# Optimization experiments

Hardware: AMD Instinct MI355X
Metric: run time of the kernel (lower is better)

The kernel has to match this reference:

```python
import jax, jax.numpy as jnp
import numpy as np

GROUPS = 8
EPS = 1e-5


def group_norm_dim1(x, gamma, beta):
    # Faithful to torch: GroupNorm treats dim 1 (height) as the channel axis.
    B, H, W, C = x.shape
    xg = x.reshape(B, GROUPS, H // GROUPS, W, C)
    mean = xg.mean(axis=(2, 3, 4), keepdims=True)
    var = xg.var(axis=(2, 3, 4), keepdims=True)
    xn = ((xg - mean) * jax.lax.rsqrt(var + EPS)).reshape(B, H, W, C)
    return xn * gamma[None, :, None, None] + beta[None, :, None, None]


def setup_inputs() -> dict:
    key = jax.random.key(0)
    ks = jax.random.split(key, 8)
    B, H, W, C = 4, 64, 64, 64  # height must equal units for GroupNorm to apply
    s = 1.0 / np.sqrt(C)
    return {
        "x": jax.random.normal(ks[0], (B, H, W, C), dtype=jnp.float32),
        "gamma": jnp.ones((C,), jnp.float32),
        "beta": jnp.zeros((C,), jnp.float32),
        "Wq": jax.random.normal(ks[1], (C, C), jnp.float32) * s,
        "bq": jnp.zeros((C,), jnp.float32),
        "Wk": jax.random.normal(ks[2], (C, C), jnp.float32) * s,
        "bk": jnp.zeros((C,), jnp.float32),
        "Wv": jax.random.normal(ks[3], (C, C), jnp.float32) * s,
        "bv": jnp.zeros((C,), jnp.float32),
        "Wo": jax.random.normal(ks[4], (C, C), jnp.float32) * s,
        "bo": jnp.zeros((C,), jnp.float32),
    }


def reference(x, gamma, beta, Wq, bq, Wk, bk, Wv, bv, Wo, bo):
    B, H, W, C = x.shape
    scale = C ** (-0.5)
    xn = group_norm_dim1(x, gamma, beta)
    q = xn @ Wq + bq
    k = xn @ Wk + bk
    v = xn @ Wv + bv
    # full spatial self-attention: scores [B, H, W, H*W]
    scores = jnp.einsum('bhwc,bijc->bhwij', q, k) * scale
    attn = jax.nn.softmax(scores.reshape(B, H, W, H * W), axis=-1)
    attn = attn.reshape(B, H, W, H, W)
    proj = jnp.einsum('bhwij,bijc->bhwc', attn, v)
    proj = proj @ Wo + bo
    return xn + proj
```

## Files before the change

### kernel.cpp

```cpp
#include <hip/hip_runtime.h>

typedef __bf16 bf16_t;
typedef bf16_t bf16x8 __attribute__((ext_vector_type(8)));
typedef bf16_t bf16x4 __attribute__((ext_vector_type(4)));
typedef short  short4v __attribute__((ext_vector_type(4)));
typedef float  f32x4  __attribute__((ext_vector_type(4)));

#define MFMA32(a, b, c) __builtin_amdgcn_mfma_f32_16x16x32_bf16(a, b, c, 0, 0, 0)
#define MFMA16(a, b, c) __builtin_amdgcn_mfma_f32_16x16x16bf16_1k(a, b, c, 0, 0, 0)

__global__ __launch_bounds__(256) void gn1w_kernel(const float* __restrict__ x,
    float2* __restrict__ partials,
    const float* __restrict__ Wq, const float* __restrict__ Wk,
    const float* __restrict__ Wv, const float* __restrict__ Wo,
    bf16_t* __restrict__ Wt) {
  int blk = blockIdx.x, t = threadIdx.x;
  if (blk >= 256) {
    int idx = (blk - 256) * 256 + t;
    int wsel = idx >> 12, rem = idx & 4095;
    int c = rem >> 6, kk = rem & 63;
    const float* src = (wsel == 0) ? Wq : ((wsel == 1) ? Wk : ((wsel == 2) ? Wv : Wo));
    Wt[idx] = (bf16_t)src[kk * 64 + c];
    return;
  }
  const float4* x4 = (const float4*)x + (size_t)blk * 1024;
  float s = 0.f, sq = 0.f;
  #pragma unroll
  for (int u = 0; u < 4; ++u) {
    float4 v = x4[u * 256 + t];
    s  += v.x + v.y + v.z + v.w;
    sq += v.x * v.x + v.y * v.y + v.z * v.z + v.w * v.w;
  }
  for (int off = 32; off; off >>= 1) {
    s  += __shfl_down(s, off, 64);
    sq += __shfl_down(sq, off, 64);
  }
  __shared__ float2 ps[4];
  if ((t & 63) == 0) ps[t >> 6] = make_float2(s, sq);
  __syncthreads();
  if (t == 0) {
    float S = 0.f, Q = 0.f;
    #pragma unroll
    for (int i = 0; i < 4; ++i) { S += ps[i].x; Q += ps[i].y; }
    partials[blk] = make_float2(S, Q);
  }
}

__global__ __launch_bounds__(256) void gnqkv_kernel(
    const float* __restrict__ x, const float* __restrict__ gamma,
    const float* __restrict__ beta, const float2* __restrict__ parts,
    const bf16_t* __restrict__ Wt,
    const float* __restrict__ bq, const float* __restrict__ bk, const float* __restrict__ bv,
    bf16_t* __restrict__ xnb, bf16_t* __restrict__ qo, bf16_t* __restrict__ ko,
    bf16_t* __restrict__ vo) {
  __shared__ __align__(16) bf16_t xl[4096];
  int blk = blockIdx.x, t = threadIdx.x;
  int grp = blk >> 3;
  float S = 0.f, Q = 0.f;
  #pragma unroll
  for (int i = 0; i < 8; ++i) { float2 p = parts[grp * 8 + i]; S += p.x; Q += p.y; }
  float mean = S * (1.f / 32768.f);
  float rstd = rsqrtf(Q * (1.f / 32768.f) - mean * mean + 1e-5f);
  int h = blk & 63;
  float ga = gamma[h] * rstd;
  float be = beta[h] - mean * ga;
  {
    int r = t >> 2, col0 = (t & 3) * 16;
    const float4* x4 = (const float4*)(x + (size_t)blk * 4096 + r * 64 + col0);
    bf16x8 pk0, pk1;
    float4 v0 = x4[0], v1 = x4[1], v2 = x4[2], v3 = x4[3];
    pk0[0] = (bf16_t)(v0.x * ga + be); pk0[1] = (bf16_t)(v0.y * ga + be);
    pk0[2] = (bf16_t)(v0.z * ga + be); pk0[3] = (bf16_t)(v0.w * ga + be);
    pk0[4] = (bf16_t)(v1.x * ga + be); pk0[5] = (bf16_t)(v1.y * ga + be);
    pk0[6] = (bf16_t)(v1.z * ga + be); pk0[7] = (bf16_t)(v1.w * ga + be);
    pk1[0] = (bf16_t)(v2.x * ga + be); pk1[1] = (bf16_t)(v2.y * ga + be);
    pk1[2] = (bf16_t)(v2.z * ga + be); pk1[3] = (bf16_t)(v2.w * ga + be);
    pk1[4] = (bf16_t)(v3.x * ga + be); pk1[5] = (bf16_t)(v3.y * ga + be);
    pk1[6] = (bf16_t)(v3.z * ga + be); pk1[7] = (bf16_t)(v3.w * ga + be);
    *(bf16x8*)&xnb[(size_t)blk * 4096 + r * 64 + col0]     = pk0;
    *(bf16x8*)&xnb[(size_t)blk * 4096 + r * 64 + col0 + 8] = pk1;
    int sw = r & 7, j0 = (t & 3) * 2;
    *(bf16x8*)&xl[r * 64 + ((j0 ^ sw) << 3)]       = pk0;
    *(bf16x8*)&xl[r * 64 + (((j0 + 1) ^ sw) << 3)] = pk1;
  }
  __syncthreads();
  int w = t >> 6, lane = t & 63, quad = lane >> 4, l16 = lane & 15;
  int rl = w * 16 + l16, sw2 = rl & 7;
  bf16x8 a0 = *(const bf16x8*)&xl[rl * 64 + ((quad ^ sw2) << 3)];
  bf16x8 a1 = *(const bf16x8*)&xl[rl * 64 + (((quad + 4) ^ sw2) << 3)];
  int m0 = blk * 64 + w * 16;
  int bi = m0 >> 12, kk0 = (m0 & 4095) + quad * 4;
  f32x4 zero = {0.f, 0.f, 0.f, 0.f};
  const float QSCALE = 0.125f * 1.44269504088896340736f;
  #pragma unroll
  for (int outk = 0; outk < 3; ++outk) {
    const bf16_t* wt = Wt + outk * 4096;
    const float* bias = (outk == 0) ? bq : ((outk == 1) ? bk : bv);
    #pragma unroll
    for (int nt = 0; nt < 4; ++nt) {
      int col = nt * 16 + l16;
      bf16x8 b0 = *(const bf16x8*)&wt[col * 64 + quad * 8];
      bf16x8 b1 = *(const bf16x8*)&wt[col * 64 + 32 + quad * 8];
      f32x4 acc = MFMA32(a0, b0, zero);
      acc = MFMA32(a1, b1, acc);
      float bb = bias[col];
      if (outk == 2) {
        bf16x4 pk;
        #pragma unroll
        for (int r = 0; r < 4; ++r) pk[r] = (bf16_t)(acc[r] + bb);
        *(bf16x4*)&vo[(size_t)bi * 262144 + (size_t)(kk0 >> 2) * 256 + col * 4] = pk;
      } else {
        #pragma unroll
        for (int r = 0; r < 4; ++r) {
          int m = m0 + quad * 4 + r;
          float v = acc[r] + bb;
          if (outk == 0) qo[(size_t)m * 64 + col] = (bf16_t)(v * QSCALE);
          else           ko[(size_t)m * 64 + col] = (bf16_t)v;
        }
      }
    }
  }
}

__global__ __launch_bounds__(256, 4) void flash_kernel(
    const bf16_t* __restrict__ q, const bf16_t* __restrict__ k,
    const bf16_t* __restrict__ vp, bf16_t* __restrict__ Opb, float* __restrict__ ml) {
  __shared__ float redO[2][2048];
  __shared__ float redL[2][128];
  int t = threadIdx.x;
  int w = t >> 6, lane = t & 63, quad = lane >> 4, l16 = lane & 15;
  int b = blockIdx.y, sp = blockIdx.z;
  int q0 = blockIdx.x * 32;

  bf16x8 qf[2][2];
  {
    const bf16_t* qp = q + ((size_t)b * 4096 + q0 + l16) * 64;
    #pragma unroll
    for (int qt = 0; qt < 2; ++qt)
      #pragma unroll
      for (int hh = 0; hh < 2; ++hh)
        qf[qt][hh] = *(const bf16x8*)&qp[qt * 1024 + hh * 32 + quad * 8];
  }
  f32x4 o[2][4];
  f32x4 zero = {0.f, 0.f, 0.f, 0.f};
  #pragma unroll
  for (int qt = 0; qt < 2; ++qt)
    #pragma unroll
    for (int ct = 0; ct < 4; ++ct) o[qt][ct] = zero;
  float rs[2] = {0.f, 0.f};

  const bf16_t* kbase = k  + (size_t)b * 262144;
  const bf16_t* vbase = vp + (size_t)b * 262144;
  int key00 = sp * 1024 + w * 256;

  bf16x8 kfA[2][2], kfB[2][2];
  #pragma unroll
  for (int kt = 0; kt < 2; ++kt)
    #pragma unroll
    for (int hh = 0; hh < 2; ++hh)
      kfA[kt][hh] = *(const bf16x8*)&kbase[(size_t)(key00 + kt * 16 + l16) * 64 + hh * 32 + quad * 8];

#define FLASH_STEP(KF, KEY0, PRE, KFN, PKEY)                                          \
  {                                                                                   \
    short4v va[4][2];                                 \
    _Pragma("unroll")                                                                 \
    for (int kt = 0; kt < 2; ++kt) {                                                  \
      int cb = (((KEY0) + kt * 16) >> 2) + quad;                                      \
      _Pragma("unroll")                                                               \
      for (int ct = 0; ct < 4; ++ct)                                                  \
        va[ct][kt] = *(const short4v*)&vbase[(size_t)cb * 256 + (ct * 16 + l16) * 4]; \
    }                                                                                 \
    if (PRE) {                                            \
      _Pragma("unroll")                                                               \
      for (int kt = 0; kt < 2; ++kt)                                                  \
        _Pragma("unroll")                                                             \
        for (int hh = 0; hh < 2; ++hh)                                                \
          KFN[kt][hh] = *(const bf16x8*)&kbase[(size_t)((PKEY) + kt * 16 + l16) * 64 + hh * 32 + quad * 8]; \
    }                                                                                 \
    _Pragma("unroll")                                                                 \
    for (int kt = 0; kt < 2; ++kt) {                                                  \
      _Pragma("unroll")                                                               \
      for (int qt = 0; qt < 2; ++qt) {                                                \
        f32x4 st = MFMA32(KF[kt][0], qf[qt][0], zero);                                \
        st = MFMA32(KF[kt][1], qf[qt][1], st);                       \
        bf16x4 pb;                                                                    \
        float psum = 0.f;                                                             \
        _Pragma("unroll")                                                             \
        for (int r = 0; r < 4; ++r) {                                                 \
          float p = __builtin_amdgcn_exp2f(st[r]);                                    \
          psum += p;                                                                  \
          pb[r] = (bf16_t)p;                                                          \
        }                                                                             \
        rs[qt] += psum;                                                               \
        short4v pshort = __builtin_bit_cast(short4v, pb);                             \
        _Pragma("unroll")                                                             \
        for (int ct = 0; ct < 4; ++ct)                                                \
          o[qt][ct] = MFMA16(va[ct][kt], pshort, o[qt][ct]);                          \
      }                                                                               \
    }                                                                                 \
  }

  #pragma unroll 1
  for (int pair = 0; pair < 4; ++pair) {
    int key0 = key00 + pair * 64;
    FLASH_STEP(kfA, key0,      1,           kfB, key0 + 32);
    FLASH_STEP(kfB, key0 + 32, (pair < 3),  kfA, key0 + 64);
  }
#undef FLASH_STEP

  #pragma unroll
  for (int qt = 0; qt < 2; ++qt) {
    rs[qt] += __shfl_xor(rs[qt], 16, 64);
    rs[qt] += __shfl_xor(rs[qt], 32, 64);
  }
  if (w >= 2) {
    int buf = w - 2;
    #pragma unroll
    for (int qt = 0; qt < 2; ++qt) {
      #pragma unroll
      for (int ct = 0; ct < 4; ++ct)
        #pragma unroll
        for (int r = 0; r < 4; ++r)
          redO[buf][((qt * 4 + ct) * 4 + r) * 64 + lane] = o[qt][ct][r];
      redL[buf][qt * 64 + lane] = rs[qt];
    }
  }
  __syncthreads();
  if (w < 2) {
    #pragma unroll
    for (int qt = 0; qt < 2; ++qt) {
      #pragma unroll
      for (int ct = 0; ct < 4; ++ct)
        #pragma unroll
        for (int r = 0; r < 4; ++r)
          o[qt][ct][r] += redO[w][((qt * 4 + ct) * 4 + r) * 64 + lane];
      rs[qt] += redL[w][qt * 64 + lane];
    }
  }
  __syncthreads();
  if (w == 1) {
    #pragma unroll
    for (int qt = 0; qt < 2; ++qt) {
      #pragma unroll
      for (int ct = 0; ct < 4; ++ct)
        #pragma unroll
        for (int r = 0; r < 4; ++r)
          redO[0][((qt * 4 + ct) * 4 + r) * 64 + lane] = o[qt][ct][r];
      redL[0][qt * 64 + lane] = rs[qt];
    }
  }
  __syncthreads();
  if (w == 0) {
    int slot = sp * 4 + b;
    #pragma unroll
    for (int qt = 0; qt < 2; ++qt) {
      float lt = rs[qt] + redL[0][qt * 64 + lane];
      if (quad == 0) ml[(size_t)slot * 4096 + q0 + qt * 16 + l16] = lt;
      #pragma unroll
      for (int ct = 0; ct < 4; ++ct) {
        bf16x4 pk;
        #pragma unroll
        for (int r = 0; r < 4; ++r)
          pk[r] = (bf16_t)(o[qt][ct][r] + redO[0][((qt * 4 + ct) * 4 + r) * 64 + lane]);
        *(bf16x4*)&Opb[((size_t)slot * 4096 + q0 + qt * 16 + l16) * 64 + ct * 16 + quad * 4] = pk;
      }
    }
  }
}

__global__ __launch_bounds__(256) void proj_kernel(
    const bf16_t* __restrict__ Opb, const float* __restrict__ ml,
    const bf16_t* __restrict__ Wt, const float* __restrict__ bo,
    const bf16_t* __restrict__ xnb, float* __restrict__ out) {
  int t = threadIdx.x, w = t >> 6, lane = t & 63, quad = lane >> 4, l16 = lane & 15;
  int blk = blockIdx.x;
  int b = blk >> 6;
  int rowb = ((blk & 63) * 64) + w * 16;
  float acc0[8], acc1[8];
  #pragma unroll
  for (int e = 0; e < 8; ++e) { acc0[e] = 0.f; acc1[e] = 0.f; }
  float lsum = 0.f;
  #pragma unroll
  for (int s = 0; s < 4; ++s) {
    size_t rr = (size_t)(s * 4 + b) * 4096 + rowb + l16;
    bf16x8 f0 = *(const bf16x8*)&Opb[rr * 64 + quad * 8];
    bf16x8 f1 = *(const bf16x8*)&Opb[rr * 64 + 32 + quad * 8];
    #pragma unroll
    for (int e = 0; e < 8; ++e) { acc0[e] += (float)f0[e]; acc1[e] += (float)f1[e]; }
    lsum += ml[rr];
  }
  float linv = 1.f / lsum;
  bf16x8 a0, a1;
  #pragma unroll
  for (int e = 0; e < 8; ++e) {
    a0[e] = (bf16_t)(acc0[e] * linv);
    a1[e] = (bf16_t)(acc1[e] * linv);
  }
  f32x4 zero = {0.f, 0.f, 0.f, 0.f};
  const bf16_t* wt = Wt + 3 * 4096;
  int m0 = blk * 64 + w * 16;
  #pragma unroll
  for (int nt = 0; nt < 4; ++nt) {
    int col = nt * 16 + l16;
    bf16x8 b0 = *(const bf16x8*)&wt[col * 64 + quad * 8];
    bf16x8 b1 = *(const bf16x8*)&wt[col * 64 + 32 + quad * 8];
    f32x4 acc = MFMA32(a0, b0, zero);
    acc = MFMA32(a1, b1, acc);
    float bb = bo[col];
    #pragma unroll
    for (int r = 0; r < 4; ++r) {
      size_t m = (size_t)m0 + quad * 4 + r;
      out[m * 64 + col] = acc[r] + bb + (float)xnb[m * 64 + col];
    }
  }
}

extern "C" void kernel_launch(void* const* d_in, const int* in_sizes, int n_in,
                              void* d_out, int out_size, void* d_ws, size_t ws_size,
                              hipStream_t stream) {
  const float* x     = (const float*)d_in[0];
  const float* gamma = (const float*)d_in[1];
  const float* beta  = (const float*)d_in[2];
  const float* Wq    = (const float*)d_in[3];
  const float* bq    = (const float*)d_in[4];
  const float* Wk    = (const float*)d_in[5];
  const float* bk    = (const float*)d_in[6];
  const float* Wv    = (const float*)d_in[7];
  const float* bv    = (const float*)d_in[8];
  const float* Wo    = (const float*)d_in[9];
  const float* bo    = (const float*)d_in[10];
  float* out = (float*)d_out;

  char* ws = (char*)d_ws;
  bf16_t* xnb   = (bf16_t*)(ws + 0);
  bf16_t* qb    = (bf16_t*)(ws + (2u  << 20));
  bf16_t* kb    = (bf16_t*)(ws + (4u  << 20));
  bf16_t* vb    = (bf16_t*)(ws + (6u  << 20));
  bf16_t* Opb   = (bf16_t*)(ws + (8u  << 20));
  float*  ml    = (float*)(ws + (16u << 20));
  float2* parts = (float2*)(ws + (17u << 20));
  bf16_t* Wt    = (bf16_t*)(ws + (17u << 20) + 4096);

  hipLaunchKernelGGL(gn1w_kernel,  dim3(320),       dim3(256), 0, stream, x, parts, Wq, Wk, Wv, Wo, Wt);
  hipLaunchKernelGGL(gnqkv_kernel, dim3(256),       dim3(256), 0, stream, x, gamma, beta, parts, Wt, bq, bk, bv, xnb, qb, kb, vb);
  hipLaunchKernelGGL(flash_kernel, dim3(128, 4, 4), dim3(256), 0, stream, qb, kb, vb, Opb, ml);
  hipLaunchKernelGGL(proj_kernel,  dim3(256),       dim3(256), 0, stream, Opb, ml, Wt, bo, xnb, out);
}
```

Before: 146.1 us.

## Fuse output projection into flash kernel and drop key-split partial buffers

Removes the split over key ranges across blocks (grid z=4). Each block now walks all 4096 keys, with each of its four waves covering 1024 keys, and the waves are reduced in LDS. The Wo projection, bias and residual add are then done inside the flash kernel, which eliminates proj_kernel, the Opb/ml intermediate buffers and one launch. V fragments are now prefetched a step ahead together with K, and launch bounds are relaxed to 2 blocks per SIMD. The trade-off is only 512 blocks, each with a 4x longer serial loop, so there is less parallelism to hide latency and more register pressure.

```diff
diff --git a/kernel.cpp b/kernel.cpp
--- a/kernel.cpp
+++ b/kernel.cpp
@@ -122,14 +122,16 @@
   }
 }
 
-__global__ __launch_bounds__(256, 4) void flash_kernel(
+__global__ __launch_bounds__(256, 2) void flash_kernel(
     const bf16_t* __restrict__ q, const bf16_t* __restrict__ k,
-    const bf16_t* __restrict__ vp, bf16_t* __restrict__ Opb, float* __restrict__ ml) {
+    const bf16_t* __restrict__ vp, const bf16_t* __restrict__ Wt,
+    const float* __restrict__ bo, const bf16_t* __restrict__ xnb,
+    float* __restrict__ out) {
   __shared__ float redO[2][2048];
   __shared__ float redL[2][128];
   int t = threadIdx.x;
   int w = t >> 6, lane = t & 63, quad = lane >> 4, l16 = lane & 15;
-  int b = blockIdx.y, sp = blockIdx.z;
+  int b = blockIdx.y;
   int q0 = blockIdx.x * 32;
 
   bf16x8 qf[2][2];
@@ -151,31 +153,34 @@
 
   const bf16_t* kbase = k  + (size_t)b * 262144;
   const bf16_t* vbase = vp + (size_t)b * 262144;
-  int key00 = sp * 1024 + w * 256;
+  int key00 = w * 1024;
 
   bf16x8 kfA[2][2], kfB[2][2];
-  #pragma unroll
-  for (int kt = 0; kt < 2; ++kt)
+  short4v vaA[4][2], vaB[4][2];
+  #pragma unroll
+  for (int kt = 0; kt < 2; ++kt) {
     #pragma unroll
     for (int hh = 0; hh < 2; ++hh)
       kfA[kt][hh] = *(const bf16x8*)&kbase[(size_t)(key00 + kt * 16 + l16) * 64 + hh * 32 + quad * 8];
-
-#define FLASH_STEP(KF, KEY0, PRE, KFN, PKEY)                                          \
+    int cb = ((key00 + kt * 16) >> 2) + quad;
+    #pragma unroll
+    for (int ct = 0; ct < 4; ++ct)
+      vaA[ct][kt] = *(const short4v*)&vbase[(size_t)cb * 256 + (ct * 16 + l16) * 4];
+  }
+
+#define FLASH_STEP(KF, VA, PRE, KFN, VAN, PKEY)                                       \
   {                                                                                   \
-    short4v va[4][2];                                 \
-    _Pragma("unroll")                                                                 \
-    for (int kt = 0; kt < 2; ++kt) {                                                  \
-      int cb = (((KEY0) + kt * 16) >> 2) + quad;                                      \
+    if (PRE) {                                      \
       _Pragma("unroll")                                                               \
-      for (int ct = 0; ct < 4; ++ct)                                                  \
-        va[ct][kt] = *(const short4v*)&vbase[(size_t)cb * 256 + (ct * 16 + l16) * 4]; \
-    }                                                                                 \
-    if (PRE) {                                            \
-      _Pragma("unroll")                                                               \
-      for (int kt = 0; kt < 2; ++kt)                                                  \
+      for (int kt = 0; kt < 2; ++kt) {                                                \
         _Pragma("unroll")                                                             \
         for (int hh = 0; hh < 2; ++hh)                                                \
           KFN[kt][hh] = *(const bf16x8*)&kbase[(size_t)((PKEY) + kt * 16 + l16) * 64 + hh * 32 + quad * 8]; \
+        int cb = (((PKEY) + kt * 16) >> 2) + quad;                                    \
+        _Pragma("unroll")                                                             \
+        for (int ct = 0; ct < 4; ++ct)                                                \
+          VAN[ct][kt] = *(const short4v*)&vbase[(size_t)cb * 256 + (ct * 16 + l16) * 4]; \
+      }                                                                               \
     }                                                                                 \
     _Pragma("unroll")                                                                 \
     for (int kt = 0; kt < 2; ++kt) {                                                  \
@@ -195,16 +200,16 @@
         short4v pshort = __builtin_bit_cast(short4v, pb);                             \
         _Pragma("unroll")                                                             \
         for (int ct = 0; ct < 4; ++ct)                                                \
-          o[qt][ct] = MFMA16(va[ct][kt], pshort, o[qt][ct]);                          \
+          o[qt][ct] = MFMA16(VA[ct][kt], pshort, o[qt][ct]);                          \
       }                                                                               \
     }                                                                                 \
   }
 
   #pragma unroll 1
-  for (int pair = 0; pair < 4; ++pair) {
+  for (int pair = 0; pair < 16; ++pair) {
     int key0 = key00 + pair * 64;
-    FLASH_STEP(kfA, key0,      1,           kfB, key0 + 32);
-    FLASH_STEP(kfB, key0 + 32, (pair < 3),  kfA, key0 + 64);
+    FLASH_STEP(kfA, vaA, 1,           kfB, vaB, key0 + 32);
+    FLASH_STEP(kfB, vaB, (pair < 15), kfA, vaA, key0 + 64);
   }
 #undef FLASH_STEP
 
@@ -238,79 +243,52 @@
     }
   }
   __syncthreads();
-  if (w == 1) {
-    #pragma unroll
-    for (int qt = 0; qt < 2; ++qt) {
-      #pragma unroll
-      for (int ct = 0; ct < 4; ++ct)
-        #pragma unroll
-        for (int r = 0; r < 4; ++r)
-          redO[0][((qt * 4 + ct) * 4 + r) * 64 + lane] = o[qt][ct][r];
-      redL[0][qt * 64 + lane] = rs[qt];
-    }
-  }
-  __syncthreads();
   if (w == 0) {
-    int slot = sp * 4 + b;
-    #pragma unroll
-    for (int qt = 0; qt < 2; ++qt) {
-      float lt = rs[qt] + redL[0][qt * 64 + lane];
-      if (quad == 0) ml[(size_t)slot * 4096 + q0 + qt * 16 + l16] = lt;
+    #pragma unroll
+    for (int ct = 0; ct < 4; ++ct)
+      #pragma unroll
+      for (int r = 0; r < 4; ++r)
+        redO[0][(ct * 4 + r) * 64 + lane] = o[1][ct][r];
+    redL[0][lane] = rs[1];
+  } else if (w == 1) {
+    #pragma unroll
+    for (int ct = 0; ct < 4; ++ct)
+      #pragma unroll
+      for (int r = 0; r < 4; ++r)
+        redO[1][(ct * 4 + r) * 64 + lane] = o[0][ct][r];
+    redL[1][lane] = rs[0];
+  }
+  __syncthreads();
+  if (w < 2) {
+    int myqt = w, ob = w ^ 1;
+    float lt = rs[myqt] + redL[ob][lane];
+    float linv = 1.f / lt;
+    short4v obf[4];
+    #pragma unroll
+    for (int ct = 0; ct < 4; ++ct) {
+      bf16x4 tb;
+      #pragma unroll
+      for (int r = 0; r < 4; ++r)
+        tb[r] = (bf16_t)((o[myqt][ct][r] + redO[ob][(ct * 4 + r) * 64 + lane]) * linv);
+      obf[ct] = __builtin_bit_cast(short4v, tb);
+    }
+    const bf16_t* wt3 = Wt + 3 * 4096;
+    int qg = b * 4096 + q0 + myqt * 16 + l16;
+    #pragma unroll
+    for (int cpt = 0; cpt < 4; ++cpt) {
+      f32x4 acc = zero;
       #pragma unroll
       for (int ct = 0; ct < 4; ++ct) {
-        bf16x4 pk;
-        #pragma unroll
-        for (int r = 0; r < 4; ++r)
-          pk[r] = (bf16_t)(o[qt][ct][r] + redO[0][((qt * 4 + ct) * 4 + r) * 64 + lane]);
-        *(bf16x4*)&Opb[((size_t)slot * 4096 + q0 + qt * 16 + l16) * 64 + ct * 16 + quad * 4] = pk;
+        short4v wa = *(const short4v*)&wt3[(cpt * 16 + l16) * 64 + ct * 16 + quad * 4];
+        acc = MFMA16(wa, obf[ct], acc);
       }
-    }
-  }
-}
-
-__global__ __launch_bounds__(256) void proj_kernel(
-    const bf16_t* __restrict__ Opb, const float* __restrict__ ml,
-    const bf16_t* __restrict__ Wt, const float* __restrict__ bo,
-    const bf16_t* __restrict__ xnb, float* __restrict__ out) {
-  int t = threadIdx.x, w = t >> 6, lane = t & 63, quad = lane >> 4, l16 = lane & 15;
-  int blk = blockIdx.x;
-  int b = blk >> 6;
-  int rowb = ((blk & 63) * 64) + w * 16;
-  float acc0[8], acc1[8];
-  #pragma unroll
-  for (int e = 0; e < 8; ++e) { acc0[e] = 0.f; acc1[e] = 0.f; }
-  float lsum = 0.f;
-  #pragma unroll
-  for (int s = 0; s < 4; ++s) {
-    size_t rr = (size_t)(s * 4 + b) * 4096 + rowb + l16;
-    bf16x8 f0 = *(const bf16x8*)&Opb[rr * 64 + quad * 8];
-    bf16x8 f1 = *(const bf16x8*)&Opb[rr * 64 + 32 + quad * 8];
-    #pragma unroll
-    for (int e = 0; e < 8; ++e) { acc0[e] += (float)f0[e]; acc1[e] += (float)f1[e]; }
-    lsum += ml[rr];
-  }
-  float linv = 1.f / lsum;
-  bf16x8 a0, a1;
-  #pragma unroll
-  for (int e = 0; e < 8; ++e) {
-    a0[e] = (bf16_t)(acc0[e] * linv);
-    a1[e] = (bf16_t)(acc1[e] * linv);
-  }
-  f32x4 zero = {0.f, 0.f, 0.f, 0.f};
-  const bf16_t* wt = Wt + 3 * 4096;
-  int m0 = blk * 64 + w * 16;
-  #pragma unroll
-  for (int nt = 0; nt < 4; ++nt) {
-    int col = nt * 16 + l16;
-    bf16x8 b0 = *(const bf16x8*)&wt[col * 64 + quad * 8];
-    bf16x8 b1 = *(const bf16x8*)&wt[col * 64 + 32 + quad * 8];
-    f32x4 acc = MFMA32(a0, b0, zero);
-    acc = MFMA32(a1, b1, acc);
-    float bb = bo[col];
-    #pragma unroll
-    for (int r = 0; r < 4; ++r) {
-      size_t m = (size_t)m0 + quad * 4 + r;
-      out[m * 64 + col] = acc[r] + bb + (float)xnb[m * 64 + col];
+      int c0 = cpt * 16 + quad * 4;
+      #pragma unroll
+      for (int r = 0; r < 4; ++r) {
+        int cc = c0 + r;
+        size_t off = (size_t)qg * 64 + cc;
+        out[off] = acc[r] + bo[cc] + (float)xnb[off];
+      }
     }
   }
 }
@@ -336,13 +314,10 @@
   bf16_t* qb    = (bf16_t*)(ws + (2u  << 20));
   bf16_t* kb    = (bf16_t*)(ws + (4u  << 20));
   bf16_t* vb    = (bf16_t*)(ws + (6u  << 20));
-  bf16_t* Opb   = (bf16_t*)(ws + (8u  << 20));
-  float*  ml    = (float*)(ws + (16u << 20));
-  float2* parts = (float2*)(ws + (17u << 20));
-  bf16_t* Wt    = (bf16_t*)(ws + (17u << 20) + 4096);
-
-  hipLaunchKernelGGL(gn1w_kernel,  dim3(320),       dim3(256), 0, stream, x, parts, Wq, Wk, Wv, Wo, Wt);
-  hipLaunchKernelGGL(gnqkv_kernel, dim3(256),       dim3(256), 0, stream, x, gamma, beta, parts, Wt, bq, bk, bv, xnb, qb, kb, vb);
-  hipLaunchKernelGGL(flash_kernel, dim3(128, 4, 4), dim3(256), 0, stream, qb, kb, vb, Opb, ml);
-  hipLaunchKernelGGL(proj_kernel,  dim3(256),       dim3(256), 0, stream, Opb, ml, Wt, bo, xnb, out);
+  float2* parts = (float2*)(ws + (8u  << 20));
+  bf16_t* Wt    = (bf16_t*)(ws + (8u  << 20) + 4096);
+
+  hipLaunchKernelGGL(gn1w_kernel,  dim3(320),    dim3(256), 0, stream, x, parts, Wq, Wk, Wv, Wo, Wt);
+  hipLaunchKernelGGL(gnqkv_kernel, dim3(256),    dim3(256), 0, stream, x, gamma, beta, parts, Wt, bq, bk, bv, xnb, qb, kb, vb);
+  hipLaunchKernelGGL(flash_kernel, dim3(128, 4), dim3(256), 0, stream, qb, kb, vb, Wt, bo, xnb, out);
 }
```

Measured after the change: 141.2 us. 3.4% less time.
